# Optimization experiments

Hardware: AMD Instinct MI355X
Metric: run time of the kernel (lower is better)

## Reference

```python
import jax, jax.numpy as jnp
import numpy as np

B, S, DIM = 2, 2048, 4096
H, KV, HD = 32, 8, 128
REP = H // KV
SCALE = HD ** -0.5
ROPE_THETA = 10000.0


def setup_inputs() -> dict:
    key = jax.random.key(0)
    ks = jax.random.split(key, 6)
    x = jax.random.normal(ks[0], (B, S, DIM), dtype=jnp.float32)
    # weights stored [in, out]; y = x @ W matches nn.Linear(in,out,bias=False)
    wq = jax.random.normal(ks[1], (DIM, H * HD), dtype=jnp.float32) * (DIM ** -0.5)
    wk = jax.random.normal(ks[2], (DIM, KV * HD), dtype=jnp.float32) * (DIM ** -0.5)
    wv = jax.random.normal(ks[3], (DIM, KV * HD), dtype=jnp.float32) * (DIM ** -0.5)
    wo = jax.random.normal(ks[4], (H * HD, DIM), dtype=jnp.float32) * ((H * HD) ** -0.5)
    # RoPE tables: angle[t, j] = t * theta^(-2j/hd)
    inv_freq = 1.0 / (ROPE_THETA ** (np.arange(0, HD, 2, dtype=np.float32) / HD))
    t = np.arange(S, dtype=np.float32)
    angles = np.outer(t, inv_freq)  # [S, HD/2]
    freqs_cos = jnp.asarray(np.cos(angles), dtype=jnp.float32)
    freqs_sin = jnp.asarray(np.sin(angles), dtype=jnp.float32)
    # causal additive mask
    neg = jnp.finfo(jnp.float32).min
    mask = jnp.where(jnp.tril(jnp.ones((S, S), dtype=bool)), 0.0, neg).astype(jnp.float32)
    positions = jnp.arange(S, dtype=jnp.int64)
    return {"x": x, "wq": wq, "wk": wk, "wv": wv, "wo": wo,
            "freqs_cos": freqs_cos, "freqs_sin": freqs_sin,
            "mask": mask, "positions": positions}


def _rope(t, cos, sin):
    # t: [b, s, h, hd]; cos/sin: [s, hd/2]
    b, s, h, hd = t.shape
    tr = t.reshape(b, s, h, hd // 2, 2)
    tre, tim = tr[..., 0], tr[..., 1]
    c = cos[None, :, None, :]
    sn = sin[None, :, None, :]
    out_re = tre * c - tim * sn
    out_im = tre * sn + tim * c
    return jnp.stack([out_re, out_im], axis=-1).reshape(b, s, h, hd)


def reference(x, wq, wk, wv, wo, freqs_cos, freqs_sin, mask, positions):
    b, s, _ = x.shape
    xq = (x @ wq).reshape(b, s, H, HD)
    xk = (x @ wk).reshape(b, s, KV, HD)
    xv = (x @ wv).reshape(b, s, KV, HD)
    xq = _rope(xq, freqs_cos, freqs_sin)
    xk = _rope(xk, freqs_cos, freqs_sin)
    # GQA without materializing repeated KV: group query heads by kv head
    q = xq.transpose(0, 2, 1, 3).reshape(b, KV, REP, s, HD)  # [b,g,r,s,d]
    k = xk.transpose(0, 2, 1, 3)                              # [b,g,s,d]
    v = xv.transpose(0, 2, 1, 3)                              # [b,g,s,d]
    scores = jnp.einsum('bgrqd,bgkd->bgrqk', q, k) * SCALE
    scores = scores + mask[None, None, None, :, :]
    probs = jax.nn.softmax(scores.astype(jnp.float32), axis=-1).astype(q.dtype)
    out = jnp.einsum('bgrqk,bgkd->bgrqd', probs, v)           # [b,g,r,s,d]
    out = out.reshape(b, H, s, HD).transpose(0, 2, 1, 3).reshape(b, s, H * HD)
    return out @ wo
```

## Files before the change

kernel.cpp:

```cpp
#include <hip/hip_runtime.h>
#include <math.h>

#define B_ 2
#define S_ 2048
#define DIM_ 4096
#define H_ 32
#define KV_ 8
#define HD_ 128
#define SCALE_ 0.08838834764831844f
#define QSCALE_ 0.12751744154254998f
#define KVOFF_ 4194304

typedef unsigned short u16;
typedef __attribute__((ext_vector_type(8))) short bf16x8;
typedef __attribute__((ext_vector_type(4))) float f32x4;
typedef __attribute__((ext_vector_type(16))) float f32x16;
typedef __attribute__((ext_vector_type(8))) unsigned short u16x8;
typedef __attribute__((ext_vector_type(4))) unsigned short u16x4;

__device__ __forceinline__ u16 f2b(float f) {
  union { float f; unsigned u; } v; v.f = f;
  unsigned r = v.u + 0x7fffu + ((v.u >> 16) & 1u);
  return (u16)(r >> 16);
}
__device__ __forceinline__ float b2f(u16 h) {
  union { unsigned u; float f; } v; v.u = ((unsigned)h) << 16;
  return v.f;
}
__device__ __forceinline__ unsigned cvt_pk_bf16(float lo, float hi) {
  unsigned r;
  asm("v_cvt_pk_bf16_f32 %0, %1, %2" : "=v"(r) : "v"(lo), "v"(hi));
  return r;
}
__device__ __forceinline__ void async_copy16(const void* g, void* l) {
  __builtin_amdgcn_global_load_lds(
      (const __attribute__((address_space(1))) void*)g,
      (__attribute__((address_space(3))) void*)l, 16, 0, 0);
}
__device__ __forceinline__ void bar() {
  asm volatile("s_barrier" ::: "memory");
}

__global__ __launch_bounds__(256) void cvt_bf16(const float* __restrict__ in,
                                                u16* __restrict__ out, int n4) {
  int i = blockIdx.x * 256 + threadIdx.x;
  if (i >= n4) return;
  float4 v = ((const float4*)in)[i];
  u16x4 o; o[0] = f2b(v.x); o[1] = f2b(v.y); o[2] = f2b(v.z); o[3] = f2b(v.w);
  ((u16x4*)out)[i] = o;
}

__global__ __launch_bounds__(256) void transpose_cvt(
    const float* __restrict__ W, u16* __restrict__ WT, int K, int N) {
  __shared__ float Ts[64][65];
  const int tid = threadIdx.x;
  const int n0 = blockIdx.x * 64, k0 = blockIdx.y * 64;
#pragma unroll
  for (int p = 0; p < 4; ++p) {
    int r = p * 16 + (tid >> 4), c = (tid & 15) * 4;
    float4 v = *(const float4*)(W + (size_t)(k0 + r) * N + n0 + c);
    Ts[r][c] = v.x; Ts[r][c + 1] = v.y; Ts[r][c + 2] = v.z; Ts[r][c + 3] = v.w;
  }
  __syncthreads();
#pragma unroll
  for (int p = 0; p < 4; ++p) {
    int n = p * 16 + (tid >> 4), kq = (tid & 15) * 4;
    u16x4 o;
    o[0] = f2b(Ts[kq + 0][n]); o[1] = f2b(Ts[kq + 1][n]);
    o[2] = f2b(Ts[kq + 2][n]); o[3] = f2b(Ts[kq + 3][n]);
    *(u16x4*)(WT + (size_t)(n0 + n) * K + k0 + kq) = o;
  }
}

__global__ __launch_bounds__(256) void transpose_v(const u16* __restrict__ V,
                                                   u16* __restrict__ Vt) {
  __shared__ u16 Ts[64][72];
  const int tid = threadIdx.x;
  const int s0 = blockIdx.x * 64, d0 = blockIdx.y * 64, hb = blockIdx.z;
  const u16* src = V + ((size_t)hb * S_ + s0) * HD_ + d0;
#pragma unroll
  for (int p = 0; p < 2; ++p) {
    int r = p * 32 + (tid >> 3), seg = (tid & 7) * 8;
    u16x8 v = *(const u16x8*)(src + (size_t)r * HD_ + seg);
#pragma unroll
    for (int j = 0; j < 8; ++j) Ts[r][seg + j] = v[j];
  }
  __syncthreads();
  u16* dst = Vt + ((size_t)hb * HD_ + d0) * S_ + s0;
#pragma unroll
  for (int p = 0; p < 2; ++p) {
    int d = p * 32 + (tid >> 3), seg = (tid & 7) * 8;
    u16x8 o;
#pragma unroll
    for (int j = 0; j < 8; ++j) o[j] = Ts[seg + j][d];
    *(u16x8*)(dst + (size_t)d * S_ + seg) = o;
  }
}

__global__ __launch_bounds__(256) void rope_bf16(unsigned* __restrict__ T,
                                                 const float* __restrict__ cs,
                                                 const float* __restrict__ sn,
                                                 int total, float scale) {
  int idx = blockIdx.x * 256 + threadIdx.x;
  if (idx >= total) return;
  int i = idx & 63, s = (idx >> 6) & (S_ - 1);
  float c = cs[s * 64 + i], si = sn[s * 64 + i];
  unsigned v = T[idx];
  float re = b2f((u16)(v & 0xffffu)), im = b2f((u16)(v >> 16));
  float ore = (re * c - im * si) * scale, oim = (re * si + im * c) * scale;
  T[idx] = (unsigned)f2b(ore) | ((unsigned)f2b(oim) << 16);
}

template <int OUT_MODE>
__global__ __launch_bounds__(256) void gemm_bf16(
    const u16* __restrict__ A, const u16* __restrict__ Bt,
    void* __restrict__ Cout, int M, int N, int K, int heads) {
  __shared__ u16 As[128 * 64];
  __shared__ u16 Bs[128 * 64];
  const int tid = threadIdx.x, lane = tid & 63;
  const int wbase = tid & ~63;
  const int o = blockIdx.y * gridDim.x + blockIdx.x;
  const int q8 = (gridDim.x * gridDim.y) >> 3;
  const int p = (o & 7) * q8 + (o >> 3);
  const int row0 = (p / gridDim.x) * 128, col0 = (p % gridDim.x) * 128;
  const int wm = ((tid >> 6) >> 1) * 64, wn = ((tid >> 6) & 1) * 64;

  f32x4 acc[4][4];
#pragma unroll
  for (int i = 0; i < 4; ++i)
#pragma unroll
    for (int j = 0; j < 4; ++j) acc[i][j] = (f32x4){0.f, 0.f, 0.f, 0.f};

  const int nk = K >> 6;
  for (int kt = 0; kt < nk; ++kt) {
    const int k0 = kt << 6;
#pragma unroll
    for (int i = 0; i < 4; ++i) {
      int g = i * 256 + tid;
      int r = g >> 3, ss = (g & 7) ^ (r & 7);
      async_copy16(A + (size_t)(row0 + r) * K + k0 + ss * 8,
                   (char*)As + (i * 256 + wbase) * 16);
    }
#pragma unroll
    for (int i = 0; i < 4; ++i) {
      int g = i * 256 + tid;
      int r = g >> 3, ss = (g & 7) ^ (r & 7);
      async_copy16(Bt + (size_t)(col0 + r) * K + k0 + ss * 8,
                   (char*)Bs + (i * 256 + wbase) * 16);
    }
    __syncthreads();
#pragma unroll
    for (int ks = 0; ks < 2; ++ks) {
      bf16x8 af[4], bf[4];
#pragma unroll
      for (int mi = 0; mi < 4; ++mi) {
        int r = wm + mi * 16 + (lane & 15);
        int off = (ks * 64 + ((lane >> 4) << 4)) ^ ((r & 7) << 4);
        af[mi] = *(const bf16x8*)((const char*)As + r * 128 + off);
      }
#pragma unroll
      for (int ni = 0; ni < 4; ++ni) {
        int r = wn + ni * 16 + (lane & 15);
        int off = (ks * 64 + ((lane >> 4) << 4)) ^ ((r & 7) << 4);
        bf[ni] = *(const bf16x8*)((const char*)Bs + r * 128 + off);
      }
#pragma unroll
      for (int mi = 0; mi < 4; ++mi)
#pragma unroll
        for (int ni = 0; ni < 4; ++ni)
          acc[mi][ni] = __builtin_amdgcn_mfma_f32_16x16x32_bf16(
              af[mi], bf[ni], acc[mi][ni], 0, 0, 0);
    }
    __syncthreads();
  }

#pragma unroll
  for (int mi = 0; mi < 4; ++mi)
#pragma unroll
    for (int ni = 0; ni < 4; ++ni) {
      int mb = row0 + wm + mi * 16 + ((lane >> 4) << 2);
      int n = col0 + wn + ni * 16 + (lane & 15);
#pragma unroll
      for (int r = 0; r < 4; ++r) {
        int m = mb + r;
        float v = acc[mi][ni][r];
        if (OUT_MODE == 0) {
          ((float*)Cout)[(size_t)m * N + n] = v;
        } else if (OUT_MODE == 1) {
          int b = m >> 11, s = m & (S_ - 1);
          int h = n >> 7, d = n & (HD_ - 1);
          ((u16*)Cout)[(((size_t)(b * heads + h)) * S_ + s) * HD_ + d] = f2b(v);
        } else {
          int b = m >> 11, s = m & (S_ - 1);
          int hh = n >> 7, d = n & (HD_ - 1);
          size_t base = (size_t)(hh >> 3) * KVOFF_;
          ((u16*)Cout)[base + (((size_t)(b * 8 + (hh & 7))) * S_ + s) * HD_ + d] =
              f2b(v);
        }
      }
    }
}

template <int OUT_MODE>
__global__ __launch_bounds__(512) void gemm256(
    const u16* __restrict__ A, const u16* __restrict__ Bt,
    void* __restrict__ Cout, int M, int N, int K, int heads) {
  __shared__ u16 lds[65536];
  char* const ldsb = (char*)lds;
  const int tid = threadIdx.x, lane = tid & 63, wid = tid >> 6;
  const int q = lane & 15, g = lane >> 4;
  const int wm = wid >> 2, wn = wid & 3;
  const int o = blockIdx.y * gridDim.x + blockIdx.x;
  const int q8 = (gridDim.x * gridDim.y) >> 3;
  const int p = (o & 7) * q8 + (o >> 3);
  const int row0 = (p / gridDim.x) * 256, col0 = (p % gridDim.x) * 256;
  const int nk = K >> 6, nh = nk << 2;

  const u16* srcA[2];
  const u16* srcB[2];
#pragma unroll
  for (int u = 0; u < 2; ++u) {
    int j = u * 512 + tid;
    int row = ((j >> 3) << 1) + ((j >> 2) & 1);
    int colg = (j & 3) ^ ((j >> 3) & 3);
    srcA[u] = A + (size_t)(row0 + row) * K + colg * 8;
    srcB[u] = Bt + (size_t)(col0 + row) * K + colg * 8;
  }

  auto STAGE = [&](int h) {
    if (h >= nh) return;
    int tau = h >> 2, ks = (h >> 1) & 1, op = h & 1;
    int slot = (2 * tau + ks) & 3;
    int koff = tau * 64 + ks * 32;
    char* lbase = ldsb + op * 65536 + slot * 16384 + wid * 1024;
#pragma unroll
    for (int u = 0; u < 2; ++u)
      async_copy16((op ? srcB[u] : srcA[u]) + koff, lbase + u * 8192);
  };

  int aread[8], bread[4];
#pragma unroll
  for (int mi = 0; mi < 8; ++mi) {
    int row = wm * 128 + mi * 16 + q;
    aread[mi] = (row >> 1) * 128 + (row & 1) * 64 + ((g ^ ((row >> 1) & 3)) << 4);
  }
#pragma unroll
  for (int ni = 0; ni < 4; ++ni) {
    int row = wn * 64 + ni * 16 + q;
    bread[ni] = (row >> 1) * 128 + (row & 1) * 64 + ((g ^ ((row >> 1) & 3)) << 4);
  }

  f32x4 acc[8][4];
#pragma unroll
  for (int i = 0; i < 8; ++i)
#pragma unroll
    for (int j = 0; j < 4; ++j) acc[i][j] = (f32x4){0.f, 0.f, 0.f, 0.f};

#pragma unroll
  for (int h = 0; h < 6; ++h) STAGE(h);
  asm volatile("s_waitcnt vmcnt(4)" ::: "memory");
  bar();

  for (int t = 0; t < nk; ++t) {
    const int s0 = (2 * t) & 3, s1 = (2 * t + 1) & 3;
    const char* As0 = ldsb + s0 * 16384;
    const char* Bs0 = ldsb + 65536 + s0 * 16384;
    const char* As1 = ldsb + s1 * 16384;
    const char* Bs1 = ldsb + 65536 + s1 * 16384;
    bf16x8 af[4], bfr[4];

#pragma unroll
    for (int i = 0; i < 4; ++i) af[i] = *(const bf16x8*)(As0 + aread[i]);
#pragma unroll
    for (int i = 0; i < 4; ++i) bfr[i] = *(const bf16x8*)(Bs0 + bread[i]);
    STAGE(4 * t + 6);
    bar();
    __builtin_amdgcn_s_setprio(1);
#pragma unroll
    for (int mi = 0; mi < 4; ++mi)
#pragma unroll
      for (int ni = 0; ni < 4; ++ni)
        acc[mi][ni] = __builtin_amdgcn_mfma_f32_16x16x32_bf16(
            af[mi], bfr[ni], acc[mi][ni], 0, 0, 0);
    __builtin_amdgcn_s_setprio(0);
    bar();

#pragma unroll
    for (int i = 0; i < 4; ++i) af[i] = *(const bf16x8*)(As0 + aread[4 + i]);
    STAGE(4 * t + 7);
    bar();
    __builtin_amdgcn_s_setprio(1);
#pragma unroll
    for (int mi = 0; mi < 4; ++mi)
#pragma unroll
      for (int ni = 0; ni < 4; ++ni)
        acc[4 + mi][ni] = __builtin_amdgcn_mfma_f32_16x16x32_bf16(
            af[mi], bfr[ni], acc[4 + mi][ni], 0, 0, 0);
    __builtin_amdgcn_s_setprio(0);
    bar();

#pragma unroll
    for (int i = 0; i < 4; ++i) af[i] = *(const bf16x8*)(As1 + aread[i]);
#pragma unroll
    for (int i = 0; i < 4; ++i) bfr[i] = *(const bf16x8*)(Bs1 + bread[i]);
    STAGE(4 * t + 8);
    bar();
    __builtin_amdgcn_s_setprio(1);
#pragma unroll
    for (int mi = 0; mi < 4; ++mi)
#pragma unroll
      for (int ni = 0; ni < 4; ++ni)
        acc[mi][ni] = __builtin_amdgcn_mfma_f32_16x16x32_bf16(
            af[mi], bfr[ni], acc[mi][ni], 0, 0, 0);
    __builtin_amdgcn_s_setprio(0);
    bar();

#pragma unroll
    for (int i = 0; i < 4; ++i) af[i] = *(const bf16x8*)(As1 + aread[4 + i]);
    STAGE(4 * t + 9);
    bar();
    __builtin_amdgcn_s_setprio(1);
#pragma unroll
    for (int mi = 0; mi < 4; ++mi)
#pragma unroll
      for (int ni = 0; ni < 4; ++ni)
        acc[4 + mi][ni] = __builtin_amdgcn_mfma_f32_16x16x32_bf16(
            af[mi], bfr[ni], acc[4 + mi][ni], 0, 0, 0);
    __builtin_amdgcn_s_setprio(0);
    if (t < nk - 2)
      asm volatile("s_waitcnt vmcnt(4)" ::: "memory");
    else if (t == nk - 2)
      asm volatile("s_waitcnt vmcnt(0)" ::: "memory");
    bar();
  }

#pragma unroll
  for (int mi = 0; mi < 8; ++mi)
#pragma unroll
    for (int ni = 0; ni < 4; ++ni) {
      int mb = row0 + wm * 128 + mi * 16 + (g << 2);
      int n = col0 + wn * 64 + ni * 16 + q;
#pragma unroll
      for (int r = 0; r < 4; ++r) {
        int m = mb + r;
        float v = acc[mi][ni][r];
        if (OUT_MODE == 0) {
          ((float*)Cout)[(size_t)m * N + n] = v;
        } else {
          int b = m >> 11, s = m & (S_ - 1);
          int h = n >> 7, d = n & (HD_ - 1);
          ((u16*)Cout)[(((size_t)(b * heads + h)) * S_ + s) * HD_ + d] = f2b(v);
        }
      }
    }
}

__global__ __launch_bounds__(256, 2) void attn_mfma(
    const u16* __restrict__ Qb, const u16* __restrict__ Kb,
    const u16* __restrict__ Vt, u16* __restrict__ AO,
    const float* __restrict__ fc, const float* __restrict__ fs) {
  __shared__ u16 Ks[64 * 128];
  __shared__ u16 Vs[128 * 64];

  const int tid = threadIdx.x, lane = tid & 63, wid = tid >> 6;
  const int wbase = tid & ~63;
  const int o = blockIdx.x + (blockIdx.y << 3) + (blockIdx.z << 8);
  const int pid = o >> 6, h = o & 31, b = (o >> 5) & 1;
  const int kvh = h >> 2;
  const int l31 = lane & 31, hi = lane >> 5;

  const u16* Kbase = Kb + ((size_t)(b * KV_ + kvh) * S_) * HD_;
  const u16* Vbase = Vt + ((size_t)(b * KV_ + kvh) * HD_) * S_;

  const u16* Kl[4];
  const u16* Vl[4];
#pragma unroll
  for (int i = 0; i < 4; ++i) {
    int gg = i * 256 + tid;
    int rK = gg >> 4, ssK = (gg & 15) ^ (rK & 7);
    Kl[i] = Kbase + (size_t)rK * HD_ + ssK * 8;
    int rV = gg >> 3, ssV = (gg & 7) ^ (rV & 7);
    Vl[i] = Vbase + (size_t)rV * S_ + ssV * 8;
  }

  for (int half = 0; half < 2; ++half) {
    const int qt = half ? (15 - pid) : pid;
    const int q0 = qt * 128;
    const int qg = q0 + wid * 32 + l31;

    bf16x8 qf[8];
    {
      const u16* qrow = Qb + ((size_t)(b * H_ + h) * S_ + qg) * HD_ + hi * 8;
      const float* cb = fc + qg * 64 + hi * 4;
      const float* sb = fs + qg * 64 + hi * 4;
#pragma unroll
      for (int ks = 0; ks < 8; ++ks) {
        u16x8 v = *(const u16x8*)(qrow + ks * 16);
        float4 cv = *(const float4*)(cb + ks * 8);
        float4 sv = *(const float4*)(sb + ks * 8);
        unsigned w[4];
#pragma unroll
        for (int j = 0; j < 4; ++j) {
          float c = ((const float*)&cv)[j] * QSCALE_;
          float s = ((const float*)&sv)[j] * QSCALE_;
          float re = b2f((u16)v[2 * j]), im = b2f((u16)v[2 * j + 1]);
          w[j] = cvt_pk_bf16(re * c - im * s, re * s + im * c);
        }
        union { unsigned u[4]; bf16x8 q; } cvt;
        cvt.u[0] = w[0]; cvt.u[1] = w[1]; cvt.u[2] = w[2]; cvt.u[3] = w[3];
        qf[ks] = cvt.q;
      }
    }

    f32x16 oacc[4];
#pragma unroll
    for (int i = 0; i < 4; ++i)
#pragma unroll
      for (int j = 0; j < 16; ++j) oacc[i][j] = 0.f;
    float mrow = -3e38f, lrow = 0.f;

    const int nkt = 2 * qt + 2;
    for (int kt = 0; kt < nkt; ++kt) {
      const int kv0 = kt * 64;
#pragma unroll
      for (int i = 0; i < 4; ++i)
        async_copy16(Kl[i] + (size_t)kv0 * HD_, (char*)Ks + (i * 256 + wbase) * 16);
#pragma unroll
      for (int i = 0; i < 4; ++i)
        async_copy16(Vl[i] + kv0, (char*)Vs + (i * 256 + wbase) * 16);
      __syncthreads();

      f32x16 sacc[2];
#pragma unroll
      for (int kf = 0; kf < 2; ++kf)
#pragma unroll
        for (int j = 0; j < 16; ++j) sacc[kf][j] = 0.f;
#pragma unroll
      for (int ks = 0; ks < 8; ++ks) {
#pragma unroll
        for (int kf = 0; kf < 2; ++kf) {
          const int arow = kf * 32 + l31;
          bf16x8 kfrag = *(const bf16x8*)(
              (const char*)Ks + arow * 256 + ((((ks * 2 + hi) << 4)) ^ ((arow & 7) << 4)));
          sacc[kf] = __builtin_amdgcn_mfma_f32_32x32x16_bf16(kfrag, qf[ks],
                                                             sacc[kf], 0, 0, 0);
        }
      }

      if (kv0 + 63 > q0 + wid * 32) {
#pragma unroll
        for (int kf = 0; kf < 2; ++kf)
#pragma unroll
          for (int r = 0; r < 16; ++r) {
            int kg = kv0 + kf * 32 + (r & 3) + 8 * (r >> 2) + 4 * hi;
            if (kg > qg) sacc[kf][r] = -3e38f;
          }
      }

      float rmax = -3e38f;
#pragma unroll
      for (int kf = 0; kf < 2; ++kf)
#pragma unroll
        for (int r = 0; r < 16; ++r) rmax = fmaxf(rmax, sacc[kf][r]);
      rmax = fmaxf(rmax, __shfl_xor(rmax, 32, 64));
      const bool defer = __all(rmax - mrow <= 11.5f);
      float mnew, fsc;
      if (defer) {
        mnew = mrow; fsc = 1.0f;
      } else {
        mnew = fmaxf(mrow, rmax); fsc = exp2f(mrow - mnew);
      }
      mrow = mnew;
      float psum = 0.f;
#pragma unroll
      for (int kf = 0; kf < 2; ++kf)
#pragma unroll
        for (int r = 0; r < 16; ++r) {
          float p = exp2f(sacc[kf][r] - mnew);
          sacc[kf][r] = p;
          psum += p;
        }
      psum += __shfl_xor(psum, 32, 64);
      lrow = lrow * fsc + psum;

      if (!defer) {
#pragma unroll
        for (int r = 0; r < 16; ++r) {
          float fr = __shfl(fsc, (r & 3) + 8 * (r >> 2) + 4 * hi, 64);
#pragma unroll
          for (int df = 0; df < 4; ++df) oacc[df][r] *= fr;
        }
      }

      bf16x8 pa[4];
#pragma unroll
      for (int kf = 0; kf < 2; ++kf) {
        unsigned w0 = cvt_pk_bf16(sacc[kf][0], sacc[kf][1]);
        unsigned w1 = cvt_pk_bf16(sacc[kf][2], sacc[kf][3]);
        unsigned w2 = cvt_pk_bf16(sacc[kf][4], sacc[kf][5]);
        unsigned w3 = cvt_pk_bf16(sacc[kf][6], sacc[kf][7]);
        unsigned w4 = cvt_pk_bf16(sacc[kf][8], sacc[kf][9]);
        unsigned w5 = cvt_pk_bf16(sacc[kf][10], sacc[kf][11]);
        unsigned w6 = cvt_pk_bf16(sacc[kf][12], sacc[kf][13]);
        unsigned w7 = cvt_pk_bf16(sacc[kf][14], sacc[kf][15]);
        asm volatile("v_permlane32_swap_b32 %0, %1" : "+v"(w0), "+v"(w2));
        asm volatile("v_permlane32_swap_b32 %0, %1" : "+v"(w1), "+v"(w3));
        asm volatile("v_permlane32_swap_b32 %0, %1" : "+v"(w4), "+v"(w6));
        asm volatile("v_permlane32_swap_b32 %0, %1" : "+v"(w5), "+v"(w7));
        union { unsigned u[4]; bf16x8 q; } f0, f1;
        f0.u[0] = w0; f0.u[1] = w1; f0.u[2] = w2; f0.u[3] = w3;
        f1.u[0] = w4; f1.u[1] = w5; f1.u[2] = w6; f1.u[3] = w7;
        pa[kf * 2] = f0.q;
        pa[kf * 2 + 1] = f1.q;
      }

#pragma unroll
      for (int ks = 0; ks < 4; ++ks) {
#pragma unroll
        for (int df = 0; df < 4; ++df) {
          const int vrow = df * 32 + l31;
          bf16x8 vf = *(const bf16x8*)(
              (const char*)Vs + vrow * 128 + ((((ks * 2 + hi) << 4)) ^ ((vrow & 7) << 4)));
          oacc[df] = __builtin_amdgcn_mfma_f32_32x32x16_bf16(pa[ks], vf,
                                                             oacc[df], 0, 0, 0);
        }
      }
      __syncthreads();
    }

    const float linv = 1.f / lrow;
#pragma unroll
    for (int r = 0; r < 16; ++r) {
      const int qloc = (r & 3) + 8 * (r >> 2) + 4 * hi;
      const float invq = __shfl(linv, qloc, 64);
      const int sq = q0 + wid * 32 + qloc;
      u16* dst = AO + (size_t)(b * S_ + sq) * (H_ * HD_) + h * HD_ + l31;
#pragma unroll
      for (int df = 0; df < 4; ++df) dst[df * 32] = f2b(oacc[df][r] * invq);
    }
  }
}

extern "C" void kernel_launch(void* const* d_in, const int* in_sizes, int n_in,
                              void* d_out, int out_size, void* d_ws, size_t ws_size,
                              hipStream_t stream) {
  const float* x  = (const float*)d_in[0];
  const float* wq = (const float*)d_in[1];
  const float* wk = (const float*)d_in[2];
  const float* wv = (const float*)d_in[3];
  const float* wo = (const float*)d_in[4];
  const float* fc = (const float*)d_in[5];
  const float* fs = (const float*)d_in[6];
  float* out = (float*)d_out;

  u16* ws  = (u16*)d_ws;
  u16* wqT = ws;
  u16* VtB = ws;
  u16* xb  = ws + 16777216;
  u16* AOb = xb;
  u16* woT = ws + 33554432;
  u16* Qh  = ws + 50331648;
  u16* wkT = ws + 67108864;
  u16* wvT = ws + 71303168;
  u16* Kh  = ws + 75497472;
  u16* Vh  = ws + 79691776;

  dim3 blk(256);

  cvt_bf16<<<dim3(16384), blk, 0, stream>>>(x, xb, 4194304);
  transpose_cvt<<<dim3(64, 64), blk, 0, stream>>>(wq, wqT, DIM_, H_ * HD_);
  transpose_cvt<<<dim3(16, 64), blk, 0, stream>>>(wk, wkT, DIM_, KV_ * HD_);
  transpose_cvt<<<dim3(16, 64), blk, 0, stream>>>(wv, wvT, DIM_, KV_ * HD_);
  transpose_cvt<<<dim3(64, 64), blk, 0, stream>>>(wo, woT, H_ * HD_, DIM_);

  gemm256<1><<<dim3(16, 16), dim3(512), 0, stream>>>(xb, wqT, Qh, 4096, 4096, 4096, H_);
  gemm_bf16<2><<<dim3(16, 32), blk, 0, stream>>>(xb, wkT, Kh, 4096, 2048, 4096, KV_);

  rope_bf16<<<dim3(8192), blk, 0, stream>>>((unsigned*)Kh, fc, fs, 2097152, 1.0f);

  transpose_v<<<dim3(32, 2, 16), blk, 0, stream>>>(Vh, VtB);

  attn_mfma<<<dim3(8, 32, 2), blk, 0, stream>>>(Qh, Kh, VtB, AOb, fc, fs);

  gemm256<0><<<dim3(16, 16), dim3(512), 0, stream>>>(AOb, woT, out, 4096, 4096, 4096, 0);
}
```

Baseline: 515.5 us.

## Double-buffer attention K/V tiles and prefetch GEMM LDS fragments

The attention kernel now keeps two LDS buffers for K and V. It issues the async copy for the next key tile before computing on the current one, so global loads overlap the QK/PV MFMA work instead of stalling at the start of each tile. In the GEMM main loop, LDS fragment reads for the next MFMA group move ahead of the barrier, right after the current MFMAs, using ping-pong register fragments. This aims to hide LDS read latency behind matrix math. The cost is double the attention LDS footprint and more live registers in the GEMM. The next-stage reads at the end of each GEMM iteration happen before the block barrier, which may race with other waves' async copies.

```diff
diff --git a/kernel.cpp b/kernel.cpp
--- a/kernel.cpp
+++ b/kernel.cpp
@@ -256,81 +256,71 @@
 #pragma unroll
     for (int j = 0; j < 4; ++j) acc[i][j] = (f32x4){0.f, 0.f, 0.f, 0.f};
 
+  auto RDA = [&](bf16x8* d, const char* s, int ob) {
+#pragma unroll
+    for (int i = 0; i < 4; ++i) d[i] = *(const bf16x8*)(s + aread[ob + i]);
+  };
+  auto RDB = [&](bf16x8* d, const char* s) {
+#pragma unroll
+    for (int i = 0; i < 4; ++i) d[i] = *(const bf16x8*)(s + bread[i]);
+  };
+  auto MFMA16 = [&](int mo, bf16x8* af, bf16x8* bfr) {
+    __builtin_amdgcn_s_setprio(1);
+#pragma unroll
+    for (int mi = 0; mi < 4; ++mi)
+#pragma unroll
+      for (int ni = 0; ni < 4; ++ni)
+        acc[mo + mi][ni] = __builtin_amdgcn_mfma_f32_16x16x32_bf16(
+            af[mi], bfr[ni], acc[mo + mi][ni], 0, 0, 0);
+    __builtin_amdgcn_s_setprio(0);
+  };
+
 #pragma unroll
   for (int h = 0; h < 6; ++h) STAGE(h);
   asm volatile("s_waitcnt vmcnt(4)" ::: "memory");
   bar();
+  bf16x8 afc[4], afn[4], bfc[4], bfn[4];
+  RDA(afc, ldsb, 0);
+  RDB(bfc, ldsb + 65536);
 
   for (int t = 0; t < nk; ++t) {
     const int s0 = (2 * t) & 3, s1 = (2 * t + 1) & 3;
     const char* As0 = ldsb + s0 * 16384;
-    const char* Bs0 = ldsb + 65536 + s0 * 16384;
+    const char* Bs1 = ldsb + 65536 + s1 * 16384;
     const char* As1 = ldsb + s1 * 16384;
-    const char* Bs1 = ldsb + 65536 + s1 * 16384;
-    bf16x8 af[4], bfr[4];
-
-#pragma unroll
-    for (int i = 0; i < 4; ++i) af[i] = *(const bf16x8*)(As0 + aread[i]);
-#pragma unroll
-    for (int i = 0; i < 4; ++i) bfr[i] = *(const bf16x8*)(Bs0 + bread[i]);
+
     STAGE(4 * t + 6);
     bar();
-    __builtin_amdgcn_s_setprio(1);
-#pragma unroll
-    for (int mi = 0; mi < 4; ++mi)
-#pragma unroll
-      for (int ni = 0; ni < 4; ++ni)
-        acc[mi][ni] = __builtin_amdgcn_mfma_f32_16x16x32_bf16(
-            af[mi], bfr[ni], acc[mi][ni], 0, 0, 0);
-    __builtin_amdgcn_s_setprio(0);
-    bar();
-
-#pragma unroll
-    for (int i = 0; i < 4; ++i) af[i] = *(const bf16x8*)(As0 + aread[4 + i]);
+    MFMA16(0, afc, bfc);
+    RDA(afn, As0, 4);
+    bar();
+
     STAGE(4 * t + 7);
     bar();
-    __builtin_amdgcn_s_setprio(1);
-#pragma unroll
-    for (int mi = 0; mi < 4; ++mi)
-#pragma unroll
-      for (int ni = 0; ni < 4; ++ni)
-        acc[4 + mi][ni] = __builtin_amdgcn_mfma_f32_16x16x32_bf16(
-            af[mi], bfr[ni], acc[4 + mi][ni], 0, 0, 0);
-    __builtin_amdgcn_s_setprio(0);
-    bar();
-
-#pragma unroll
-    for (int i = 0; i < 4; ++i) af[i] = *(const bf16x8*)(As1 + aread[i]);
-#pragma unroll
-    for (int i = 0; i < 4; ++i) bfr[i] = *(const bf16x8*)(Bs1 + bread[i]);
+    MFMA16(4, afn, bfc);
+    RDA(afc, As1, 0);
+    RDB(bfn, Bs1);
+    bar();
+
     STAGE(4 * t + 8);
     bar();
-    __builtin_amdgcn_s_setprio(1);
-#pragma unroll
-    for (int mi = 0; mi < 4; ++mi)
-#pragma unroll
-      for (int ni = 0; ni < 4; ++ni)
-        acc[mi][ni] = __builtin_amdgcn_mfma_f32_16x16x32_bf16(
-            af[mi], bfr[ni], acc[mi][ni], 0, 0, 0);
-    __builtin_amdgcn_s_setprio(0);
-    bar();
-
-#pragma unroll
-    for (int i = 0; i < 4; ++i) af[i] = *(const bf16x8*)(As1 + aread[4 + i]);
+    MFMA16(0, afc, bfn);
+    RDA(afn, As1, 4);
+    bar();
+
     STAGE(4 * t + 9);
     bar();
-    __builtin_amdgcn_s_setprio(1);
-#pragma unroll
-    for (int mi = 0; mi < 4; ++mi)
-#pragma unroll
-      for (int ni = 0; ni < 4; ++ni)
-        acc[4 + mi][ni] = __builtin_amdgcn_mfma_f32_16x16x32_bf16(
-            af[mi], bfr[ni], acc[4 + mi][ni], 0, 0, 0);
-    __builtin_amdgcn_s_setprio(0);
+    MFMA16(4, afn, bfn);
     if (t < nk - 2)
       asm volatile("s_waitcnt vmcnt(4)" ::: "memory");
     else if (t == nk - 2)
       asm volatile("s_waitcnt vmcnt(0)" ::: "memory");
+    if (t < nk - 1) {
+      const char* As0n = ldsb + ((2 * t + 2) & 3) * 16384;
+      const char* Bs0n = ldsb + 65536 + ((2 * t + 2) & 3) * 16384;
+      RDA(afc, As0n, 0);
+      RDB(bfc, Bs0n);
+    }
     bar();
   }
 
@@ -359,8 +349,8 @@
     const u16* __restrict__ Qb, const u16* __restrict__ Kb,
     const u16* __restrict__ Vt, u16* __restrict__ AO,
     const float* __restrict__ fc, const float* __restrict__ fs) {
-  __shared__ u16 Ks[64 * 128];
-  __shared__ u16 Vs[128 * 64];
+  __shared__ u16 Ks[2][64 * 128];
+  __shared__ u16 Vs[2][128 * 64];
 
   const int tid = threadIdx.x, lane = tid & 63, wid = tid >> 6;
   const int wbase = tid & ~63;
@@ -383,10 +373,23 @@
     Vl[i] = Vbase + (size_t)rV * S_ + ssV * 8;
   }
 
+  auto STAGE_KV = [&](int kt, int buf) {
+    const int kv0 = kt * 64;
+#pragma unroll
+    for (int i = 0; i < 4; ++i)
+      async_copy16(Kl[i] + (size_t)kv0 * HD_,
+                   (char*)Ks[buf] + (i * 256 + wbase) * 16);
+#pragma unroll
+    for (int i = 0; i < 4; ++i)
+      async_copy16(Vl[i] + kv0, (char*)Vs[buf] + (i * 256 + wbase) * 16);
+  };
+
   for (int half = 0; half < 2; ++half) {
     const int qt = half ? (15 - pid) : pid;
     const int q0 = qt * 128;
     const int qg = q0 + wid * 32 + l31;
+
+    STAGE_KV(0, 0);
 
     bf16x8 qf[8];
     {
@@ -419,16 +422,15 @@
       for (int j = 0; j < 16; ++j) oacc[i][j] = 0.f;
     float mrow = -3e38f, lrow = 0.f;
 
+    __syncthreads();
+
     const int nkt = 2 * qt + 2;
     for (int kt = 0; kt < nkt; ++kt) {
+      const int cur = kt & 1;
+      if (kt + 1 < nkt) STAGE_KV(kt + 1, cur ^ 1);
+      const char* Kc = (const char*)Ks[cur];
+      const char* Vc = (const char*)Vs[cur];
       const int kv0 = kt * 64;
-#pragma unroll
-      for (int i = 0; i < 4; ++i)
-        async_copy16(Kl[i] + (size_t)kv0 * HD_, (char*)Ks + (i * 256 + wbase) * 16);
-#pragma unroll
-      for (int i = 0; i < 4; ++i)
-        async_copy16(Vl[i] + kv0, (char*)Vs + (i * 256 + wbase) * 16);
-      __syncthreads();
 
       f32x16 sacc[2];
 #pragma unroll
@@ -441,7 +443,7 @@
         for (int kf = 0; kf < 2; ++kf) {
           const int arow = kf * 32 + l31;
           bf16x8 kfrag = *(const bf16x8*)(
-              (const char*)Ks + arow * 256 + ((((ks * 2 + hi) << 4)) ^ ((arow & 7) << 4)));
+              Kc + arow * 256 + ((((ks * 2 + hi) << 4)) ^ ((arow & 7) << 4)));
           sacc[kf] = __builtin_amdgcn_mfma_f32_32x32x16_bf16(kfrag, qf[ks],
                                                              sacc[kf], 0, 0, 0);
         }
@@ -520,7 +522,7 @@
         for (int df = 0; df < 4; ++df) {
           const int vrow = df * 32 + l31;
           bf16x8 vf = *(const bf16x8*)(
-              (const char*)Vs + vrow * 128 + ((((ks * 2 + hi) << 4)) ^ ((vrow & 7) << 4)));
+              Vc + vrow * 128 + ((((ks * 2 + hi) << 4)) ^ ((vrow & 7) << 4)));
           oacc[df] = __builtin_amdgcn_mfma_f32_32x32x16_bf16(pa[ks], vf,
                                                              oacc[df], 0, 0, 0);
         }
```

New measurement: 517.6 us. Within noise of the previous version (+0.4%).
